# Kernel optimization log

Measured on AMD Instinct MI355X. Metric: run time of the kernel, lower is better.

Reference implementation:

```python
import jax, jax.numpy as jnp
import numpy as np

B, S, E, H = 2, 2048, 512, 8
D = E // H  # head_dim = 64


def setup_inputs() -> dict:
    key = jax.random.key(0)
    ks = jax.random.split(key, 10)
    sc = 1.0 / np.sqrt(E)
    x = jax.random.normal(ks[0], (B, S, E), dtype=jnp.float32)
    # parent index per node: tree_structure[b][parent[b,i]] contains i
    parent = jax.random.randint(ks[1], (B, S), 0, S, dtype=jnp.int32)
    Wp = jax.random.normal(ks[2], (E, E), dtype=jnp.float32) * sc
    bp = jnp.zeros((E,), dtype=jnp.float32)
    Wc = jax.random.normal(ks[3], (E, E), dtype=jnp.float32) * sc
    bc = jnp.zeros((E,), dtype=jnp.float32)
    Ws = jax.random.normal(ks[4], (E, E), dtype=jnp.float32) * sc
    bs = jnp.zeros((E,), dtype=jnp.float32)
    Wo = jax.random.normal(ks[5], (E, E), dtype=jnp.float32) * sc
    bo = jnp.zeros((E,), dtype=jnp.float32)
    return {"x": x, "parent": parent, "Wp": Wp, "bp": bp, "Wc": Wc,
            "bc": bc, "Ws": Ws, "bs": bs, "Wo": Wo, "bo": bo}


def _tree_mask(parent):
    # Vectorized equivalent of the per-batch scatter loop:
    # mask[b, p, c] = mask[b, c, p] = 1 for each (parent, child) edge.
    b_idx = jnp.arange(B)[:, None]
    rows = jnp.arange(S)[None, :]
    m = jnp.zeros((B, S, S), dtype=bool)
    m = m.at[b_idx, rows, parent].set(True)
    m = m.at[b_idx, parent, rows].set(True)
    return m  # (B, S, S), broadcast over heads


def reference(x, parent, Wp, bp, Wc, bc, Ws, bs, Wo, bo):
    # Tri-projection
    p = (x @ Wp + bp).reshape(B, S, H, D)
    c = (x @ Wc + bc).reshape(B, S, H, D)
    s = (x @ Ws + bs).reshape(B, S, H, D)
    scores = jnp.einsum('bnhd,bmhd->bnhm', p, c) / jnp.sqrt(jnp.float32(D))
    mask = _tree_mask(parent)  # (B, S, S)
    scores = jnp.where(mask[:, :, None, :], scores, -jnp.inf)
    attn = jax.nn.softmax(scores, axis=-1)  # dropout is identity (train=False)
    out = jnp.einsum('bnhm,bmhd->bnhd', attn, s).reshape(B, S, E)
    return out @ Wo + bo
```

## Files before the change

kernel.cpp:

```cpp
#include <hip/hip_runtime.h>
#include <hip/hip_bf16.h>

#define B_  2
#define S_  2048
#define E_  512
#define H_  8
#define D_  64
#define BS_ (B_ * S_)
#define N1_ 1536
#define K_  512

typedef __bf16 bf16x8 __attribute__((ext_vector_type(8)));
typedef float  f32x4  __attribute__((ext_vector_type(4)));
typedef unsigned short us8 __attribute__((ext_vector_type(8)));

__device__ __forceinline__ ushort f2bf(float f) {
    unsigned u = __float_as_uint(f);
    unsigned r = (u + 0x7FFFu + ((u >> 16) & 1u)) >> 16;
    return (ushort)r;
}
__device__ __forceinline__ float bf2f(ushort b) {
    return __uint_as_float(((unsigned)b) << 16);
}

__device__ __forceinline__ void gld_lds16(const ushort* g, ushort* l) {
    __builtin_amdgcn_global_load_lds(
        (const __attribute__((address_space(1))) unsigned int*)g,
        (__attribute__((address_space(3))) unsigned int*)l, 16, 0, 0);
}

__global__ __launch_bounds__(256) void prep_kernel(
    const float* __restrict__ x, ushort* __restrict__ xb,
    const float* __restrict__ Wp, const float* __restrict__ Wc,
    const float* __restrict__ Ws, const float* __restrict__ Wo,
    ushort* __restrict__ Wcat_t, ushort* __restrict__ Wo_t) {
    int bid = blockIdx.x;
    int tid = threadIdx.x;
    if (bid < 2048) {
        int i = bid * 256 + tid;
        float4 v = ((const float4*)x)[i];
        ushort4 o;
        o.x = f2bf(v.x); o.y = f2bf(v.y); o.z = f2bf(v.z); o.w = f2bf(v.w);
        ((ushort4*)xb)[i] = o;
        return;
    }
    __shared__ ushort T[64][65];
    int bid2 = bid - 2048;
    int z = bid2 >> 6;
    int t = bid2 & 63;
    const float* src = (z == 0) ? Wp : (z == 1) ? Wc : (z == 2) ? Ws : Wo;
    ushort* dst = (z < 3) ? (Wcat_t + (size_t)z * 512 * 512) : Wo_t;
    int n0 = (t & 7) * 64, k0 = (t >> 3) * 64;
    int g = tid >> 6, l = tid & 63;
    #pragma unroll
    for (int r = 0; r < 16; r++) {
        int kk = g * 16 + r;
        T[kk][l] = f2bf(src[(size_t)(k0 + kk) * 512 + n0 + l]);
    }
    __syncthreads();
    #pragma unroll
    for (int r = 0; r < 16; r++) {
        int nn = g * 16 + r;
        dst[(size_t)(n0 + nn) * 512 + k0 + l] = T[l][nn];
    }
}

template<int TN, bool BF16OUT>
__global__ __launch_bounds__(256) void gemm_mfma_kernel(
    const ushort* __restrict__ A,
    const ushort* __restrict__ Bt,
    const float*  __restrict__ b0,
    const float*  __restrict__ b1,
    const float*  __restrict__ b2,
    void* __restrict__ Cv,
    int N, int K) {
    constexpr int TM = 128, TK = 64;
    constexpr int NF = TN / 32;
    __shared__ ushort As[TM][TK];
    __shared__ ushort Bs[TN][TK];

    const int tid  = threadIdx.x;
    const int lane = tid & 63;
    const int wave = tid >> 6;
    const int wm = wave >> 1, wn = wave & 1;
    const int row0 = blockIdx.y * TM;
    const int col0 = blockIdx.x * TN;

    f32x4 acc[4][NF] = {};

    const int srow = lane >> 3;
    const int scol = (lane & 7) * 8;

    const int lrow = lane & 15;
    const int lk   = (lane >> 4) * 8;

    for (int kt = 0; kt < K; kt += TK) {
        const ushort* ga = A + (size_t)(row0 + wave * 32 + srow) * K + kt + scol;
        #pragma unroll
        for (int j = 0; j < 4; j++)
            gld_lds16(ga + (size_t)j * 8 * K, &As[wave * 32 + j * 8][0]);
        const ushort* gb = Bt + (size_t)(col0 + wave * (TN / 4) + srow) * K + kt + scol;
        #pragma unroll
        for (int j = 0; j < NF; j++)
            gld_lds16(gb + (size_t)j * 8 * K, &Bs[wave * (TN / 4) + j * 8][0]);
        __syncthreads();

        #pragma unroll
        for (int kk = 0; kk < TK; kk += 32) {
            bf16x8 af[4], bfr[NF];
            #pragma unroll
            for (int i = 0; i < 4; i++)
                af[i] = *(const bf16x8*)(&As[wm * 64 + i * 16 + lrow][kk + lk]);
            #pragma unroll
            for (int j = 0; j < NF; j++)
                bfr[j] = *(const bf16x8*)(&Bs[wn * (TN / 2) + j * 16 + lrow][kk + lk]);
            #pragma unroll
            for (int i = 0; i < 4; i++)
                #pragma unroll
                for (int j = 0; j < NF; j++)
                    acc[i][j] = __builtin_amdgcn_mfma_f32_16x16x32_bf16(
                        af[i], bfr[j], acc[i][j], 0, 0, 0);
        }
        __syncthreads();
    }

    const int ccol = lane & 15;
    const int crow = (lane >> 4) * 4;
    #pragma unroll
    for (int j = 0; j < NF; j++) {
        int gcol = col0 + wn * (TN / 2) + j * 16 + ccol;
        float bias = (gcol < 512) ? b0[gcol]
                   : (gcol < 1024) ? b1[gcol - 512] : b2[gcol - 1024];
        #pragma unroll
        for (int i = 0; i < 4; i++) {
            int grow = row0 + wm * 64 + i * 16 + crow;
            #pragma unroll
            for (int rg = 0; rg < 4; rg++) {
                float v = acc[i][j][rg] + bias;
                if (BF16OUT)
                    ((ushort*)Cv)[(size_t)(grow + rg) * N + gcol] = f2bf(v);
                else
                    ((float*)Cv)[(size_t)(grow + rg) * N + gcol] = v;
            }
        }
    }
}

__global__ __launch_bounds__(256) void attn_gather_kernel(
    const ushort* __restrict__ PCS, const int* __restrict__ parent,
    ushort* __restrict__ attn) {
    int gtid = blockIdx.x * blockDim.x + threadIdx.x;
    int w    = gtid >> 6;
    int lane = gtid & 63;
    int bbase = ((w >> 11) << 11);
    int i  = w & (S_ - 1);
    int rp = bbase + parent[w];

    float pnf[8];
    {
        us8 p8 = *(const us8*)(PCS + (size_t)w * N1_ + lane * 8);
        #pragma unroll
        for (int j = 0; j < 8; j++) pnf[j] = bf2f(p8[j]);
    }

    float Z, av[8];
    {
        const ushort* rm = PCS + (size_t)rp * N1_;
        us8 c8 = *(const us8*)(rm + 512  + lane * 8);
        us8 s8 = *(const us8*)(rm + 1024 + lane * 8);
        float t = 0.f;
        #pragma unroll
        for (int j = 0; j < 8; j++) t += pnf[j] * bf2f(c8[j]);
        t += __shfl_xor(t, 1); t += __shfl_xor(t, 2); t += __shfl_xor(t, 4);
        float e = __expf(t * 0.125f);
        Z = e;
        #pragma unroll
        for (int j = 0; j < 8; j++) av[j] = e * bf2f(s8[j]);
    }

    for (int t0 = 0; t0 < S_; t0 += 256) {
        int4 pv = *(const int4*)(parent + bbase + t0 + lane * 4);
        int pc[4] = {pv.x, pv.y, pv.z, pv.w};
        #pragma unroll
        for (int jj = 0; jj < 4; jj++) {
            unsigned long long mask = __ballot(pc[jj] == i);
            while (mask) {
                int l = __ffsll(mask) - 1;
                mask &= mask - 1;
                int c = bbase + t0 + l * 4 + jj;
                if (c == rp) continue;
                const ushort* rc = PCS + (size_t)c * N1_;
                us8 c8 = *(const us8*)(rc + 512  + lane * 8);
                us8 s8 = *(const us8*)(rc + 1024 + lane * 8);
                float t = 0.f;
                #pragma unroll
                for (int j = 0; j < 8; j++) t += pnf[j] * bf2f(c8[j]);
                t += __shfl_xor(t, 1); t += __shfl_xor(t, 2); t += __shfl_xor(t, 4);
                float e = __expf(t * 0.125f);
                Z += e;
                #pragma unroll
                for (int j = 0; j < 8; j++) av[j] += e * bf2f(s8[j]);
            }
        }
    }

    float rz = 1.0f / Z;
    us8 o8;
    #pragma unroll
    for (int j = 0; j < 8; j++) o8[j] = f2bf(av[j] * rz);
    *(us8*)(attn + (size_t)w * E_ + lane * 8) = o8;
}

extern "C" void kernel_launch(void* const* d_in, const int* in_sizes, int n_in,
                              void* d_out, int out_size, void* d_ws, size_t ws_size,
                              hipStream_t stream) {
    const float* x      = (const float*)d_in[0];
    const int*   parent = (const int*)  d_in[1];
    const float* Wp     = (const float*)d_in[2];
    const float* bp     = (const float*)d_in[3];
    const float* Wc     = (const float*)d_in[4];
    const float* bc     = (const float*)d_in[5];
    const float* Ws     = (const float*)d_in[6];
    const float* bs     = (const float*)d_in[7];
    const float* Wo     = (const float*)d_in[8];
    const float* bo     = (const float*)d_in[9];
    float* out = (float*)d_out;

    char* ws = (char*)d_ws;
    ushort* x_bf    = (ushort*)(ws + 0);
    ushort* Wcat_t  = (ushort*)(ws + 4194304);
    ushort* Wo_t    = (ushort*)(ws + 5767168);
    ushort* PCS_bf  = (ushort*)(ws + 6291456);
    ushort* attn_bf = (ushort*)(ws + 18874368);

    prep_kernel<<<2304, 256, 0, stream>>>(x, x_bf, Wp, Wc, Ws, Wo, Wcat_t, Wo_t);

    gemm_mfma_kernel<64, true><<<dim3(N1_ / 64, BS_ / 128), 256, 0, stream>>>(
        x_bf, Wcat_t, bp, bc, bs, PCS_bf, N1_, K_);

    attn_gather_kernel<<<BS_ * 64 / 256, 256, 0, stream>>>(
        PCS_bf, parent, attn_bf);

    gemm_mfma_kernel<64, false><<<dim3(E_ / 64, BS_ / 128), 256, 0, stream>>>(
        attn_bf, Wo_t, bo, bo, bo, out, E_, K_);
}
```

Measured before the change: 116.4 us.

## Fuse fp32-to-bf16 conversion and weight transpose into GEMM loads, drop prep kernel

Removes the separate prep kernel that converted x and the weights to bf16 and transposed the weights. Both GEMMs now read fp32 directly from global memory, convert in registers and transpose the weight tile into padded LDS. The first GEMM uses a 96-wide N tile, and the second GEMM uses 64x64 tiles so more blocks launch. This saves a kernel launch and the intermediate bf16 copies, but the GEMMs now issue synchronous fp32 loads instead of async LDS loads and repeat the conversion work in every block.

New measurement: 124.5 us. 6.9% more time.

```diff
diff --git a/kernel.cpp b/kernel.cpp
--- a/kernel.cpp
+++ b/kernel.cpp
@@ -29,55 +29,16 @@
         (__attribute__((address_space(3))) unsigned int*)l, 16, 0, 0);
 }
 
-__global__ __launch_bounds__(256) void prep_kernel(
-    const float* __restrict__ x, ushort* __restrict__ xb,
+__global__ __launch_bounds__(256) void gemm1_kernel(
+    const float* __restrict__ x,
     const float* __restrict__ Wp, const float* __restrict__ Wc,
-    const float* __restrict__ Ws, const float* __restrict__ Wo,
-    ushort* __restrict__ Wcat_t, ushort* __restrict__ Wo_t) {
-    int bid = blockIdx.x;
-    int tid = threadIdx.x;
-    if (bid < 2048) {
-        int i = bid * 256 + tid;
-        float4 v = ((const float4*)x)[i];
-        ushort4 o;
-        o.x = f2bf(v.x); o.y = f2bf(v.y); o.z = f2bf(v.z); o.w = f2bf(v.w);
-        ((ushort4*)xb)[i] = o;
-        return;
-    }
-    __shared__ ushort T[64][65];
-    int bid2 = bid - 2048;
-    int z = bid2 >> 6;
-    int t = bid2 & 63;
-    const float* src = (z == 0) ? Wp : (z == 1) ? Wc : (z == 2) ? Ws : Wo;
-    ushort* dst = (z < 3) ? (Wcat_t + (size_t)z * 512 * 512) : Wo_t;
-    int n0 = (t & 7) * 64, k0 = (t >> 3) * 64;
-    int g = tid >> 6, l = tid & 63;
-    #pragma unroll
-    for (int r = 0; r < 16; r++) {
-        int kk = g * 16 + r;
-        T[kk][l] = f2bf(src[(size_t)(k0 + kk) * 512 + n0 + l]);
-    }
-    __syncthreads();
-    #pragma unroll
-    for (int r = 0; r < 16; r++) {
-        int nn = g * 16 + r;
-        dst[(size_t)(n0 + nn) * 512 + k0 + l] = T[l][nn];
-    }
-}
-
-template<int TN, bool BF16OUT>
-__global__ __launch_bounds__(256) void gemm_mfma_kernel(
-    const ushort* __restrict__ A,
-    const ushort* __restrict__ Bt,
-    const float*  __restrict__ b0,
-    const float*  __restrict__ b1,
-    const float*  __restrict__ b2,
-    void* __restrict__ Cv,
-    int N, int K) {
-    constexpr int TM = 128, TK = 64;
-    constexpr int NF = TN / 32;
-    __shared__ ushort As[TM][TK];
-    __shared__ ushort Bs[TN][TK];
+    const float* __restrict__ Ws,
+    const float* __restrict__ bp, const float* __restrict__ bc,
+    const float* __restrict__ bs,
+    ushort* __restrict__ PCS) {
+    constexpr int TM = 128, TN = 96, TK = 64, LDP = 72;
+    __shared__ ushort As[TM][LDP];
+    __shared__ ushort Bs[TN][LDP];
 
     const int tid  = threadIdx.x;
     const int lane = tid & 63;
@@ -86,38 +47,61 @@
     const int row0 = blockIdx.y * TM;
     const int col0 = blockIdx.x * TN;
 
-    f32x4 acc[4][NF] = {};
-
-    const int srow = lane >> 3;
-    const int scol = (lane & 7) * 8;
-
+    f32x4 acc[4][3] = {};
+
+    const int ar  = tid >> 4;
+    const int ac4 = tid & 15;
     const int lrow = lane & 15;
     const int lk   = (lane >> 4) * 8;
 
-    for (int kt = 0; kt < K; kt += TK) {
-        const ushort* ga = A + (size_t)(row0 + wave * 32 + srow) * K + kt + scol;
-        #pragma unroll
-        for (int j = 0; j < 4; j++)
-            gld_lds16(ga + (size_t)j * 8 * K, &As[wave * 32 + j * 8][0]);
-        const ushort* gb = Bt + (size_t)(col0 + wave * (TN / 4) + srow) * K + kt + scol;
-        #pragma unroll
-        for (int j = 0; j < NF; j++)
-            gld_lds16(gb + (size_t)j * 8 * K, &Bs[wave * (TN / 4) + j * 8][0]);
+    for (int kt = 0; kt < K_; kt += TK) {
+        #pragma unroll
+        for (int j = 0; j < 8; j++) {
+            int row = j * 16 + ar;
+            float4 v = *(const float4*)(x + (size_t)(row0 + row) * K_ + kt + ac4 * 4);
+            ushort4 h;
+            h.x = f2bf(v.x); h.y = f2bf(v.y); h.z = f2bf(v.z); h.w = f2bf(v.w);
+            *(ushort4*)(&As[row][ac4 * 4]) = h;
+        }
+        #pragma unroll
+        for (int rd = 0; rd < 2; rd++) {
+            int pid = rd * 256 + tid;
+            if (pid < 384) {
+                int pk = pid / 24, pn = pid % 24;
+                int gc = col0 + pn * 4;
+                const float* Wseg = (gc < 512) ? (Wp + gc)
+                                  : (gc < 1024) ? (Wc + gc - 512)
+                                  : (Ws + gc - 1024);
+                float4 r0 = *(const float4*)(Wseg + (size_t)(kt + pk * 4 + 0) * 512);
+                float4 r1 = *(const float4*)(Wseg + (size_t)(kt + pk * 4 + 1) * 512);
+                float4 r2 = *(const float4*)(Wseg + (size_t)(kt + pk * 4 + 2) * 512);
+                float4 r3 = *(const float4*)(Wseg + (size_t)(kt + pk * 4 + 3) * 512);
+                ushort4 h;
+                h.x = f2bf(r0.x); h.y = f2bf(r1.x); h.z = f2bf(r2.x); h.w = f2bf(r3.x);
+                *(ushort4*)(&Bs[pn * 4 + 0][pk * 4]) = h;
+                h.x = f2bf(r0.y); h.y = f2bf(r1.y); h.z = f2bf(r2.y); h.w = f2bf(r3.y);
+                *(ushort4*)(&Bs[pn * 4 + 1][pk * 4]) = h;
+                h.x = f2bf(r0.z); h.y = f2bf(r1.z); h.z = f2bf(r2.z); h.w = f2bf(r3.z);
+                *(ushort4*)(&Bs[pn * 4 + 2][pk * 4]) = h;
+                h.x = f2bf(r0.w); h.y = f2bf(r1.w); h.z = f2bf(r2.w); h.w = f2bf(r3.w);
+                *(ushort4*)(&Bs[pn * 4 + 3][pk * 4]) = h;
+            }
+        }
         __syncthreads();
 
         #pragma unroll
         for (int kk = 0; kk < TK; kk += 32) {
-            bf16x8 af[4], bfr[NF];
+            bf16x8 af[4], bfr[3];
             #pragma unroll
             for (int i = 0; i < 4; i++)
                 af[i] = *(const bf16x8*)(&As[wm * 64 + i * 16 + lrow][kk + lk]);
             #pragma unroll
-            for (int j = 0; j < NF; j++)
-                bfr[j] = *(const bf16x8*)(&Bs[wn * (TN / 2) + j * 16 + lrow][kk + lk]);
+            for (int j = 0; j < 3; j++)
+                bfr[j] = *(const bf16x8*)(&Bs[wn * 48 + j * 16 + lrow][kk + lk]);
             #pragma unroll
             for (int i = 0; i < 4; i++)
                 #pragma unroll
-                for (int j = 0; j < NF; j++)
+                for (int j = 0; j < 3; j++)
                     acc[i][j] = __builtin_amdgcn_mfma_f32_16x16x32_bf16(
                         af[i], bfr[j], acc[i][j], 0, 0, 0);
         }
@@ -127,21 +111,97 @@
     const int ccol = lane & 15;
     const int crow = (lane >> 4) * 4;
     #pragma unroll
-    for (int j = 0; j < NF; j++) {
-        int gcol = col0 + wn * (TN / 2) + j * 16 + ccol;
-        float bias = (gcol < 512) ? b0[gcol]
-                   : (gcol < 1024) ? b1[gcol - 512] : b2[gcol - 1024];
+    for (int j = 0; j < 3; j++) {
+        int gcol = col0 + wn * 48 + j * 16 + ccol;
+        float bias = (gcol < 512) ? bp[gcol]
+                   : (gcol < 1024) ? bc[gcol - 512] : bs[gcol - 1024];
         #pragma unroll
         for (int i = 0; i < 4; i++) {
             int grow = row0 + wm * 64 + i * 16 + crow;
             #pragma unroll
-            for (int rg = 0; rg < 4; rg++) {
-                float v = acc[i][j][rg] + bias;
-                if (BF16OUT)
-                    ((ushort*)Cv)[(size_t)(grow + rg) * N + gcol] = f2bf(v);
-                else
-                    ((float*)Cv)[(size_t)(grow + rg) * N + gcol] = v;
-            }
+            for (int rg = 0; rg < 4; rg++)
+                PCS[(size_t)(grow + rg) * N1_ + gcol] = f2bf(acc[i][j][rg] + bias);
+        }
+    }
+}
+
+__global__ __launch_bounds__(256) void gemm2_kernel(
+    const ushort* __restrict__ A,
+    const float* __restrict__ Wo, const float* __restrict__ bo,
+    float* __restrict__ out) {
+    constexpr int TM = 64, TN = 64, TK = 64, LDP = 72;
+    __shared__ ushort As[TM][TK];
+    __shared__ ushort Bs[TN][LDP];
+
+    const int tid  = threadIdx.x;
+    const int lane = tid & 63;
+    const int wave = tid >> 6;
+    const int wm = wave >> 1, wn = wave & 1;
+    const int row0 = blockIdx.y * TM;
+    const int col0 = blockIdx.x * TN;
+
+    f32x4 acc[2][2] = {};
+
+    const int srow = lane >> 3;
+    const int scol = (lane & 7) * 8;
+    const int pk = tid >> 4, pn = tid & 15;
+    const int lrow = lane & 15;
+    const int lk   = (lane >> 4) * 8;
+
+    for (int kt = 0; kt < K_; kt += TK) {
+        const ushort* ga = A + (size_t)(row0 + wave * 16 + srow) * K_ + kt + scol;
+        gld_lds16(ga,            &As[wave * 16 + 0][0]);
+        gld_lds16(ga + 8 * K_,   &As[wave * 16 + 8][0]);
+
+        {
+            const float* Wseg = Wo + col0 + pn * 4;
+            float4 r0 = *(const float4*)(Wseg + (size_t)(kt + pk * 4 + 0) * 512);
+            float4 r1 = *(const float4*)(Wseg + (size_t)(kt + pk * 4 + 1) * 512);
+            float4 r2 = *(const float4*)(Wseg + (size_t)(kt + pk * 4 + 2) * 512);
+            float4 r3 = *(const float4*)(Wseg + (size_t)(kt + pk * 4 + 3) * 512);
+            ushort4 h;
+            h.x = f2bf(r0.x); h.y = f2bf(r1.x); h.z = f2bf(r2.x); h.w = f2bf(r3.x);
+            *(ushort4*)(&Bs[pn * 4 + 0][pk * 4]) = h;
+            h.x = f2bf(r0.y); h.y = f2bf(r1.y); h.z = f2bf(r2.y); h.w = f2bf(r3.y);
+            *(ushort4*)(&Bs[pn * 4 + 1][pk * 4]) = h;
+            h.x = f2bf(r0.z); h.y = f2bf(r1.z); h.z = f2bf(r2.z); h.w = f2bf(r3.z);
+            *(ushort4*)(&Bs[pn * 4 + 2][pk * 4]) = h;
+            h.x = f2bf(r0.w); h.y = f2bf(r1.w); h.z = f2bf(r2.w); h.w = f2bf(r3.w);
+            *(ushort4*)(&Bs[pn * 4 + 3][pk * 4]) = h;
+        }
+        __syncthreads();
+
+        #pragma unroll
+        for (int kk = 0; kk < TK; kk += 32) {
+            bf16x8 af[2], bfr[2];
+            #pragma unroll
+            for (int i = 0; i < 2; i++)
+                af[i] = *(const bf16x8*)(&As[wm * 32 + i * 16 + lrow][kk + lk]);
+            #pragma unroll
+            for (int j = 0; j < 2; j++)
+                bfr[j] = *(const bf16x8*)(&Bs[wn * 32 + j * 16 + lrow][kk + lk]);
+            #pragma unroll
+            for (int i = 0; i < 2; i++)
+                #pragma unroll
+                for (int j = 0; j < 2; j++)
+                    acc[i][j] = __builtin_amdgcn_mfma_f32_16x16x32_bf16(
+                        af[i], bfr[j], acc[i][j], 0, 0, 0);
+        }
+        __syncthreads();
+    }
+
+    const int ccol = lane & 15;
+    const int crow = (lane >> 4) * 4;
+    #pragma unroll
+    for (int j = 0; j < 2; j++) {
+        int gcol = col0 + wn * 32 + j * 16 + ccol;
+        float bias = bo[gcol];
+        #pragma unroll
+        for (int i = 0; i < 2; i++) {
+            int grow = row0 + wm * 32 + i * 16 + crow;
+            #pragma unroll
+            for (int rg = 0; rg < 4; rg++)
+                out[(size_t)(grow + rg) * E_ + gcol] = acc[i][j][rg] + bias;
         }
     }
 }
@@ -227,20 +287,15 @@
     float* out = (float*)d_out;
 
     char* ws = (char*)d_ws;
-    ushort* x_bf    = (ushort*)(ws + 0);
-    ushort* Wcat_t  = (ushort*)(ws + 4194304);
-    ushort* Wo_t    = (ushort*)(ws + 5767168);
-    ushort* PCS_bf  = (ushort*)(ws + 6291456);
-    ushort* attn_bf = (ushort*)(ws + 18874368);
-
-    prep_kernel<<<2304, 256, 0, stream>>>(x, x_bf, Wp, Wc, Ws, Wo, Wcat_t, Wo_t);
-
-    gemm_mfma_kernel<64, true><<<dim3(N1_ / 64, BS_ / 128), 256, 0, stream>>>(
-        x_bf, Wcat_t, bp, bc, bs, PCS_bf, N1_, K_);
+    ushort* PCS_bf  = (ushort*)(ws + 0);
+    ushort* attn_bf = (ushort*)(ws + 12582912);
+
+    gemm1_kernel<<<dim3(N1_ / 96, BS_ / 128), 256, 0, stream>>>(
+        x, Wp, Wc, Ws, bp, bc, bs, PCS_bf);
 
     attn_gather_kernel<<<BS_ * 64 / 256, 256, 0, stream>>>(
         PCS_bf, parent, attn_bf);
 
-    gemm_mfma_kernel<64, false><<<dim3(E_ / 64, BS_ / 128), 256, 0, stream>>>(
-        attn_bf, Wo_t, bo, bo, bo, out, E_, K_);
-}
+    gemm2_kernel<<<dim3(E_ / 64, BS_ / 64), 256, 0, stream>>>(
+        attn_bf, Wo, bo, out);
+}
```
